# Kernel tuning notes

Measured on AMD Instinct MI355X. Metric: run time of the kernel, lower is better.

Reference implementation:

```python
import jax, jax.numpy as jnp
import numpy as np

DIM = 2048
NUM_HEADS = 16
HEAD_DIM = DIM // NUM_HEADS
HIDDEN = 4 * DIM
EPS = 1e-6


def rmsnorm(x, w):
    # Faithful to source: weight * (x * dim**-0.5 / sqrt(mean(x^2) + eps))
    scale = DIM ** -0.5
    norm = jnp.sqrt(jnp.mean(x * x, axis=-1, keepdims=True) + EPS)
    return w * (x * scale / norm)


def setup_inputs() -> dict:
    key = jax.random.key(0)
    ks = jax.random.split(key, 10)
    def init(k, shape, fan_in):
        return jax.random.normal(k, shape, dtype=jnp.float32) * (fan_in ** -0.5)
    return {
        "x": jax.random.normal(ks[0], (2, 2048, DIM), dtype=jnp.float32),
        "norm1_w": jnp.ones((DIM,), dtype=jnp.float32),
        "wq": init(ks[1], (DIM, DIM), DIM),
        "wk": init(ks[2], (HEAD_DIM, DIM), DIM),
        "wv": init(ks[3], (HEAD_DIM, DIM), DIM),
        "wo": init(ks[4], (DIM, DIM), DIM),
        "norm2_w": jnp.ones((DIM,), dtype=jnp.float32),
        "w1": init(ks[5], (HIDDEN, DIM), DIM),
        "w2": init(ks[6], (DIM, HIDDEN), HIDDEN),
        "w3": init(ks[7], (HIDDEN, DIM), DIM),
    }


def reference(x, norm1_w, wq, wk, wv, wo, norm2_w, w1, w2, w3):
    B, S, _ = x.shape
    # --- Multi-Query Attention (pre-norm) ---
    h = rmsnorm(x, norm1_w)
    q = h @ wq.T                                  # [B,S,D]
    k = h @ wk.T                                  # [B,S,hd] (shared across heads)
    v = h @ wv.T                                  # [B,S,hd]
    q = q.reshape(B, S, NUM_HEADS, HEAD_DIM)
    # scores: q @ k^T / sqrt(hd); k is broadcast (repeated) across heads
    scores = jnp.einsum('bshd,btd->bhst', q, k) / (HEAD_DIM ** 0.5)  # [B,H,S,S]
    probs = jax.nn.softmax(scores, axis=-1)
    attn = jnp.einsum('bhst,btd->bshd', probs, v).reshape(B, S, DIM)
    x = x + attn @ wo.T
    # --- SwiGLU FFN (pre-norm) ---
    h = rmsnorm(x, norm2_w)
    ffn = (jax.nn.silu(h @ w1.T) * (h @ w3.T)) @ w2.T
    return x + ffn
```

## Files before the change

kernel.cpp:

```cpp
#include <hip/hip_runtime.h>
#include <hip/hip_bf16.h>

typedef __attribute__((ext_vector_type(4))) float f32x4;
typedef __attribute__((ext_vector_type(8))) short s16x8;
typedef __attribute__((ext_vector_type(4))) short s16x4;
typedef __attribute__((ext_vector_type(2))) short s16x2;

#define MFMA_BF16 __builtin_amdgcn_mfma_f32_16x16x32_bf16

__device__ inline short f2bf(float f) {
  unsigned u = __float_as_uint(f);
  u = (u + 0x7FFFu + ((u >> 16) & 1u)) >> 16;
  return (short)u;
}
__device__ inline float bf2f(short s) {
  return __uint_as_float(((unsigned)(unsigned short)s) << 16);
}

#define DPPF(x, ctrl) __int_as_float(__builtin_amdgcn_update_dpp( \
    __float_as_int(x), __float_as_int(x), ctrl, 0xF, 0xF, false))
__device__ inline float rowmax16(float x) {
  x = fmaxf(x, DPPF(x, 0xB1));
  x = fmaxf(x, DPPF(x, 0x4E));
  x = fmaxf(x, DPPF(x, 0x124));
  x = fmaxf(x, DPPF(x, 0x128));
  return x;
}
__device__ inline float rowsum16(float x) {
  x += DPPF(x, 0xB1);
  x += DPPF(x, 0x4E);
  x += DPPF(x, 0x124);
  x += DPPF(x, 0x128);
  return x;
}

__global__ __launch_bounds__(256) void cvt_kernel(
    const float* __restrict__ in, short* __restrict__ out, int n, float scale)
{
  int idx = (blockIdx.x * 256 + threadIdx.x) * 8;
  if (idx >= n) return;
  f32x4 a = *(const f32x4*)(in + idx);
  f32x4 b = *(const f32x4*)(in + idx + 4);
  s16x8 o;
  #pragma unroll
  for (int j = 0; j < 4; ++j) { o[j] = f2bf(a[j] * scale); o[4 + j] = f2bf(b[j] * scale); }
  *(s16x8*)(out + idx) = o;
}

__global__ __launch_bounds__(256) void rmsnorm_kernel(
    const float* __restrict__ x, const float* __restrict__ w, short* __restrict__ out)
{
  size_t row = blockIdx.x;
  const float* xr = x + row * 2048;
  int base = threadIdx.x * 8;
  f32x4 a = *(const f32x4*)(xr + base);
  f32x4 b = *(const f32x4*)(xr + base + 4);
  float ss = a[0]*a[0] + a[1]*a[1] + a[2]*a[2] + a[3]*a[3]
           + b[0]*b[0] + b[1]*b[1] + b[2]*b[2] + b[3]*b[3];
  #pragma unroll
  for (int off = 1; off < 64; off <<= 1) ss += __shfl_xor(ss, off, 64);
  __shared__ float red[4];
  if ((threadIdx.x & 63) == 0) red[threadIdx.x >> 6] = ss;
  __syncthreads();
  float tot = red[0] + red[1] + red[2] + red[3];
  float rn = rsqrtf(tot * (1.0f / 2048.0f) + 1e-6f) * 0.022097086912079608f;
  f32x4 wa = *(const f32x4*)(w + base);
  f32x4 wb = *(const f32x4*)(w + base + 4);
  s16x8 o;
  #pragma unroll
  for (int j = 0; j < 4; ++j) {
    o[j]     = f2bf(a[j] * wa[j] * rn);
    o[4 + j] = f2bf(b[j] * wb[j] * rn);
  }
  *(s16x8*)(out + row * 2048 + base) = o;
}

template <int MODE>
__global__ __launch_bounds__(256, 2) void gemm_bt_kernel(
    const short* __restrict__ A, const short* __restrict__ B,
    void* __restrict__ Cv, const float* __restrict__ resid,
    int M, int N, int K)
{
  __shared__ short As[128 * 32];
  __shared__ short Bs[128 * 32];
  int tid = threadIdx.x;
  int lane = tid & 63;
  int w = tid >> 6;
  int r = lane & 15, g = lane >> 4;
  int wr = w >> 1, wc = w & 1;
  size_t row0 = (size_t)blockIdx.y * 128;
  size_t col0 = (size_t)blockIdx.x * 128;

  f32x4 acc[4][4];
  #pragma unroll
  for (int i = 0; i < 4; ++i)
    #pragma unroll
    for (int j = 0; j < 4; ++j) acc[i][j] = (f32x4){0.f, 0.f, 0.f, 0.f};

  const short* Ablk = A + row0 * K;
  const short* Bblk = B + col0 * K;
  int arow = tid >> 2;
  int akk = (tid & 3) << 3;

  for (int k0 = 0; k0 < K; k0 += 32) {
    #pragma unroll
    for (int i = 0; i < 2; ++i) {
      int chunk = i * 256 + tid;
      int rr = i * 64 + arow;
      __builtin_amdgcn_global_load_lds(
          (const __attribute__((address_space(1))) unsigned int*)(Ablk + (size_t)rr * K + k0 + akk),
          (__attribute__((address_space(3))) unsigned int*)(&As[chunk * 8]), 16, 0, 0);
      __builtin_amdgcn_global_load_lds(
          (const __attribute__((address_space(1))) unsigned int*)(Bblk + (size_t)rr * K + k0 + akk),
          (__attribute__((address_space(3))) unsigned int*)(&Bs[chunk * 8]), 16, 0, 0);
    }
    __syncthreads();
    s16x8 af[4], bfr[4];
    #pragma unroll
    for (int mm = 0; mm < 4; ++mm)
      af[mm] = *(const s16x8*)(&As[(wr * 64 + mm * 16 + r) * 32 + g * 8]);
    #pragma unroll
    for (int nn = 0; nn < 4; ++nn)
      bfr[nn] = *(const s16x8*)(&Bs[(wc * 64 + nn * 16 + r) * 32 + g * 8]);
    #pragma unroll
    for (int mm = 0; mm < 4; ++mm)
      #pragma unroll
      for (int nn = 0; nn < 4; ++nn)
        acc[mm][nn] = MFMA_BF16(af[mm], bfr[nn], acc[mm][nn], 0, 0, 0);
    __syncthreads();
  }

  #pragma unroll
  for (int mm = 0; mm < 4; ++mm) {
    #pragma unroll
    for (int nn = 0; nn < 4; ++nn) {
      #pragma unroll
      for (int j = 0; j < 4; ++j) {
        size_t rr = row0 + wr * 64 + mm * 16 + g * 4 + j;
        size_t cc = col0 + wc * 64 + nn * 16 + r;
        size_t idx = rr * (size_t)N + cc;
        if constexpr (MODE == 0) {
          ((short*)Cv)[idx] = f2bf(acc[mm][nn][j]);
        } else if constexpr (MODE == 1) {
          ((float*)Cv)[idx] = acc[mm][nn][j] + resid[idx];
        } else {
          short* gp = (short*)Cv;
          float gv = bf2f(gp[idx]);
          float sg = gv / (1.0f + __expf(-gv));
          gp[idx] = f2bf(sg * acc[mm][nn][j]);
        }
      }
    }
  }
}


#define STAGEA(T, KH)                                                          \
  _Pragma("unroll")                                                            \
  for (int i = 0; i < 2; ++i) {                                                \
    int lc = i * 512 + tid;                                                    \
    int rw = lc >> 2, cp = lc & 3;                                             \
    __builtin_amdgcn_global_load_lds(                                          \
        (const __attribute__((address_space(1))) unsigned int*)                \
            (Ablk + (size_t)rw * K + (T) * 64 + (KH) * 32 +                    \
             ((cp ^ ((rw >> 1) & 3)) << 3)),                                   \
        (__attribute__((address_space(3))) unsigned int*)                      \
            (&As[(T) & 1][KH][lc * 8]), 16, 0, 0);                             \
  }

#define STAGEB(T, KH)                                                          \
  _Pragma("unroll")                                                            \
  for (int i = 0; i < BLOADS; ++i) {                                           \
    int lc = i * 512 + tid;                                                    \
    int rw = lc >> 2, cp = lc & 3;                                             \
    __builtin_amdgcn_global_load_lds(                                          \
        (const __attribute__((address_space(1))) unsigned int*)                \
            (Bblk + (size_t)rw * K + (T) * 64 + (KH) * 32 +                    \
             ((cp ^ ((rw >> 1) & 3)) << 3)),                                   \
        (__attribute__((address_space(3))) unsigned int*)                      \
            (&Bs[(T) & 1][KH][lc * 8]), 16, 0, 0);                             \
  }

#define LDA8(D, KH, MH)                                                        \
  _Pragma("unroll")                                                            \
  for (int mi = 0; mi < 4; ++mi) {                                             \
    int rowa = wr * 128 + ((MH) * 4 + mi) * 16 + r;                            \
    a[mi] = *(const s16x8*)(&As[D][KH][rowa * 32 + chsw * 8]);                 \
  }

#define LDB8(D, KH)                                                            \
  _Pragma("unroll")                                                            \
  for (int ni = 0; ni < NREP; ++ni) {                                          \
    int rowb = wc * WN + ni * 16 + r;                                          \
    b[ni] = *(const s16x8*)(&Bs[D][KH][rowb * 32 + chsw * 8]);                 \
  }

#define MF16(MH)                                                               \
  __builtin_amdgcn_s_setprio(1);                                               \
  _Pragma("unroll")                                                            \
  for (int mi = 0; mi < 4; ++mi)                                               \
    _Pragma("unroll")                                                          \
    for (int ni = 0; ni < NREP; ++ni)                                          \
      acc[(MH) * 4 + mi][ni] =                                                 \
          MFMA_BF16(a[mi], b[ni], acc[(MH) * 4 + mi][ni], 0, 0, 0);            \
  __builtin_amdgcn_s_setprio(0);

#define WAITC                                                                  \
  do {                                                                         \
    if constexpr (BN == 256)                                                   \
      asm volatile("s_waitcnt vmcnt(4)" ::: "memory");                         \
    else                                                                       \
      asm volatile("s_waitcnt vmcnt(3)" ::: "memory");                         \
  } while (0)

#define BAR __builtin_amdgcn_s_barrier()

template <int BN, int MODE>
__global__ __launch_bounds__(512, 2) void gemm8p_kernel(
    const short* __restrict__ A, const short* __restrict__ B,
    void* __restrict__ Cv, const float* __restrict__ resid,
    int M, int N, int K)
{
  constexpr int BLOADS = BN / 128;
  constexpr int WN = BN / 4;
  constexpr int NREP = WN / 16;
  __shared__ short As[2][2][256 * 32];
  __shared__ short Bs[2][2][BN * 32];

  int tid = threadIdx.x;
  int lane = tid & 63;
  int w = tid >> 6;
  int r = lane & 15, g = lane >> 4;
  int wr = w >> 2, wc = w & 3;
  int chsw = g ^ ((r >> 1) & 3);

  int nwg = gridDim.x * gridDim.y;
  int orig = blockIdx.y * gridDim.x + blockIdx.x;
  int swz = (orig & 7) * (nwg >> 3) + (orig >> 3);
  int bx = swz % gridDim.x, by = swz / gridDim.x;
  size_t row0 = (size_t)by * 256;
  size_t col0 = (size_t)bx * BN;

  const short* Ablk = A + row0 * K;
  const short* Bblk = B + col0 * K;

  f32x4 acc[8][NREP];
  #pragma unroll
  for (int i = 0; i < 8; ++i)
    #pragma unroll
    for (int j = 0; j < NREP; ++j) acc[i][j] = (f32x4){0.f, 0.f, 0.f, 0.f};

  s16x8 a[4], b[NREP];
  int NT = K >> 6;

  STAGEA(0, 0); STAGEB(0, 0); STAGEA(0, 1); STAGEB(0, 1);
  WAITC;
  BAR;

  for (int t = 0; t < NT; ++t) {
    int d = t & 1;
    bool nl = (t < NT - 1);
    LDA8(d, 0, 0); LDB8(d, 0);
    if (nl) { STAGEA(t + 1, 0); }
    BAR;
    MF16(0);
    BAR;
    LDA8(d, 0, 1);
    if (nl) { STAGEB(t + 1, 0); WAITC; }
    else    { asm volatile("s_waitcnt vmcnt(0)" ::: "memory"); }
    BAR;
    MF16(1);
    BAR;
    LDA8(d, 1, 0); LDB8(d, 1);
    if (nl) { STAGEA(t + 1, 1); }
    BAR;
    MF16(0);
    BAR;
    LDA8(d, 1, 1);
    if (nl) { STAGEB(t + 1, 1); WAITC; }
    BAR;
    MF16(1);
    BAR;
  }

  #pragma unroll
  for (int mi = 0; mi < 8; ++mi) {
    #pragma unroll
    for (int ni = 0; ni < NREP; ++ni) {
      #pragma unroll
      for (int j = 0; j < 4; ++j) {
        size_t rr = row0 + wr * 128 + mi * 16 + g * 4 + j;
        size_t cc = col0 + wc * WN + ni * 16 + r;
        size_t idx = rr * (size_t)N + cc;
        if constexpr (MODE == 0) {
          ((short*)Cv)[idx] = f2bf(acc[mi][ni][j]);
        } else if constexpr (MODE == 1) {
          ((float*)Cv)[idx] = acc[mi][ni][j] + resid[idx];
        } else {
          short* gp = (short*)Cv;
          float gv = bf2f(gp[idx]);
          float sg = gv / (1.0f + __expf(-gv));
          gp[idx] = f2bf(sg * acc[mi][ni][j]);
        }
      }
    }
  }
}

__global__ __launch_bounds__(256) void transpose_v_kernel(
    const short* __restrict__ kv, short* __restrict__ vt)
{
  __shared__ short t[64][65];
  int b = blockIdx.z;
  int s0 = blockIdx.x * 64;
  int d0 = blockIdx.y * 64;
  int tid = threadIdx.x;
  #pragma unroll
  for (int i = 0; i < 16; ++i) {
    int e = i * 256 + tid;
    int sr = e >> 6, dc = e & 63;
    t[sr][dc] = kv[(size_t)(b * 2048 + s0 + sr) * 256 + 128 + d0 + dc];
  }
  __syncthreads();
  #pragma unroll
  for (int i = 0; i < 16; ++i) {
    int e = i * 256 + tid;
    int dr = e >> 6, sc = e & 63;
    vt[(size_t)b * 128 * 2048 + (size_t)(d0 + dr) * 2048 + s0 + sc] = t[sc][dr];
  }
}

__global__ __launch_bounds__(256, 2) void attn_kernel(
    const short* __restrict__ q, const short* __restrict__ kv,
    const short* __restrict__ vt, short* __restrict__ out)
{
  const int S = 2048;
  int tid = threadIdx.x;
  int w = tid >> 6;
  int lane = tid & 63;
  int r = lane & 15, g = lane >> 4;
  int h = blockIdx.y, b = blockIdx.z;
  int qrow0 = blockIdx.x * 128 + w * 32;

  __shared__ short Ks[2][4096];
  __shared__ short Vs[2][4096];
  __shared__ short Ps[4][32][40];

  const short* kvsrc = kv + (size_t)b * S * 256;
  const short* vsrc  = vt + (size_t)b * 128 * S;

  const short* qbase = q + ((size_t)(b * S + qrow0 + r)) * 2048 + h * 128;
  s16x8 qa[2][4];
  #pragma unroll
  for (int gq = 0; gq < 2; ++gq)
    #pragma unroll
    for (int dc = 0; dc < 4; ++dc)
      qa[gq][dc] = *(const s16x8*)(qbase + gq * 16 * 2048 + dc * 32 + g * 8);

  f32x4 o[2][8];
  #pragma unroll
  for (int gq = 0; gq < 2; ++gq)
    #pragma unroll
    for (int dt = 0; dt < 8; ++dt) o[gq][dt] = (f32x4){0.f, 0.f, 0.f, 0.f};
  float m[2][4], l[2][4];
  #pragma unroll
  for (int gq = 0; gq < 2; ++gq)
    #pragma unroll
    for (int j = 0; j < 4; ++j) { m[gq][j] = -1e30f; l[gq][j] = 0.f; }

#define STAGE(KVT, BSEL)                                                        \
  {                                                                             \
    int kv0s = (KVT) * 32;                                                      \
    _Pragma("unroll")                                                           \
    for (int i = 0; i < 2; ++i) {                                               \
      int c = w * 64 + lane + i * 256;                                          \
      int krow = c >> 4, kcp = c & 15;                                          \
      __builtin_amdgcn_global_load_lds(                                         \
          (const __attribute__((address_space(1))) unsigned int*)               \
              (kvsrc + (size_t)(kv0s + krow) * 256 + ((kcp ^ (krow & 7)) << 3)),\
          (__attribute__((address_space(3))) unsigned int*)(&Ks[BSEL][c * 8]),  \
          16, 0, 0);                                                            \
      int vrow = c >> 2, vcp = c & 3;                                           \
      __builtin_amdgcn_global_load_lds(                                         \
          (const __attribute__((address_space(1))) unsigned int*)               \
              (vsrc + (size_t)vrow * S + kv0s + ((vcp ^ (vrow & 3)) << 3)),     \
          (__attribute__((address_space(3))) unsigned int*)(&Vs[BSEL][c * 8]),  \
          16, 0, 0);                                                            \
    }                                                                           \
  }

  STAGE(0, 0);
  __syncthreads();

  for (int it = 0; it < 64; ++it) {
    int cur = it & 1;
    if (it < 63) STAGE(it + 1, cur ^ 1);

    s16x8 kc0[4], kc1[4], vb[8];
    #pragma unroll
    for (int dc = 0; dc < 4; ++dc) {
      kc0[dc] = *(const s16x8*)(&Ks[cur][r * 128 + (((dc * 4 + g) ^ (r & 7)) << 3)]);
      kc1[dc] = *(const s16x8*)(&Ks[cur][(16 + r) * 128 + (((dc * 4 + g) ^ (r & 7)) << 3)]);
    }
    #pragma unroll
    for (int dt = 0; dt < 8; ++dt)
      vb[dt] = *(const s16x8*)(&Vs[cur][(dt * 16 + r) * 32 + ((g ^ (r & 3)) << 3)]);

    f32x4 sc0[2], sc1[2];
    #pragma unroll
    for (int gq = 0; gq < 2; ++gq) { sc0[gq] = (f32x4){0.f,0.f,0.f,0.f}; sc1[gq] = (f32x4){0.f,0.f,0.f,0.f}; }
    __builtin_amdgcn_s_setprio(1);
    #pragma unroll
    for (int dc = 0; dc < 4; ++dc) {
      #pragma unroll
      for (int gq = 0; gq < 2; ++gq) {
        sc0[gq] = MFMA_BF16(qa[gq][dc], kc0[dc], sc0[gq], 0, 0, 0);
        sc1[gq] = MFMA_BF16(qa[gq][dc], kc1[dc], sc1[gq], 0, 0, 0);
      }
    }
    __builtin_amdgcn_s_setprio(0);

    float p0[2][4], p1[2][4];
    #pragma unroll
    for (int gq = 0; gq < 2; ++gq) {
      float mx[4];
      #pragma unroll
      for (int j = 0; j < 4; ++j) mx[j] = rowmax16(fmaxf(sc0[gq][j], sc1[gq][j]));
      bool nd = (mx[0] > m[gq][0] + 8.f) | (mx[1] > m[gq][1] + 8.f)
              | (mx[2] > m[gq][2] + 8.f) | (mx[3] > m[gq][3] + 8.f);
      if (__any(nd)) {
        #pragma unroll
        for (int j = 0; j < 4; ++j) {
          float mn = fmaxf(m[gq][j], mx[j]);
          float alpha = __expf(m[gq][j] - mn);
          m[gq][j] = mn;
          l[gq][j] *= alpha;
          #pragma unroll
          for (int dt = 0; dt < 8; ++dt) o[gq][dt][j] *= alpha;
        }
      }
      #pragma unroll
      for (int j = 0; j < 4; ++j) {
        p0[gq][j] = __expf(sc0[gq][j] - m[gq][j]);
        p1[gq][j] = __expf(sc1[gq][j] - m[gq][j]);
        l[gq][j] += p0[gq][j] + p1[gq][j];
      }
      #pragma unroll
      for (int j = 0; j < 4; ++j) {
        Ps[w][gq * 16 + g * 4 + j][r]      = f2bf(p0[gq][j]);
        Ps[w][gq * 16 + g * 4 + j][16 + r] = f2bf(p1[gq][j]);
      }
    }
    asm volatile("s_waitcnt lgkmcnt(0)" ::: "memory");
    __builtin_amdgcn_sched_barrier(0);
    s16x8 pa0 = *(const s16x8*)(&Ps[w][r][g * 8]);
    s16x8 pa1 = *(const s16x8*)(&Ps[w][16 + r][g * 8]);
    __builtin_amdgcn_s_setprio(1);
    #pragma unroll
    for (int dt = 0; dt < 8; ++dt) {
      o[0][dt] = MFMA_BF16(pa0, vb[dt], o[0][dt], 0, 0, 0);
      o[1][dt] = MFMA_BF16(pa1, vb[dt], o[1][dt], 0, 0, 0);
    }
    __builtin_amdgcn_s_setprio(0);
    __syncthreads();
  }

  #pragma unroll
  for (int gq = 0; gq < 2; ++gq) {
    float linv[4];
    #pragma unroll
    for (int j = 0; j < 4; ++j) linv[j] = 1.0f / rowsum16(l[gq][j]);
    short* ob = out + ((size_t)(b * S + qrow0 + gq * 16)) * 2048 + h * 128;
    #pragma unroll
    for (int dt = 0; dt < 8; ++dt)
      #pragma unroll
      for (int j = 0; j < 4; ++j)
        ob[(size_t)(g * 4 + j) * 2048 + dt * 16 + r] = f2bf(o[gq][dt][j] * linv[j]);
  }
#undef STAGE
}

extern "C" void kernel_launch(void* const* d_in, const int* in_sizes, int n_in,
                              void* d_out, int out_size, void* d_ws, size_t ws_size,
                              hipStream_t stream) {
  const float* x   = (const float*)d_in[0];
  const float* n1w = (const float*)d_in[1];
  const float* wq  = (const float*)d_in[2];
  const float* wk  = (const float*)d_in[3];
  const float* wv  = (const float*)d_in[4];
  const float* wo  = (const float*)d_in[5];
  const float* n2w = (const float*)d_in[6];
  const float* w1  = (const float*)d_in[7];
  const float* w2  = (const float*)d_in[8];
  const float* w3  = (const float*)d_in[9];
  float* out = (float*)d_out;
  char* ws = (char*)d_ws;
  const size_t MB = 1ull << 20;
  short* wqb  = (short*)(ws);
  short* wob  = (short*)(ws + 8 * MB);
  short* w1b  = (short*)(ws + 16 * MB);
  short* w2b  = (short*)(ws + 48 * MB);
  short* w3b  = (short*)(ws + 80 * MB);
  short* wkvb = (short*)(ws + 112 * MB);
  short* h1   = (short*)(ws + 113 * MB);
  short* gbuf = (short*)(ws + 129 * MB);
  short* qb   = (short*)(ws + 129 * MB);
  short* kvb  = (short*)(ws + 145 * MB);
  short* vtb  = (short*)(ws + 147 * MB);

  const float qscale = 0.08838834764831845f;
  cvt_kernel<<<2048, 256, 0, stream>>>(wq, wqb, 4194304, qscale);
  cvt_kernel<<<128,  256, 0, stream>>>(wk, wkvb, 262144, 1.0f);
  cvt_kernel<<<128,  256, 0, stream>>>(wv, wkvb + 262144, 262144, 1.0f);
  cvt_kernel<<<2048, 256, 0, stream>>>(wo, wob, 4194304, 1.0f);
  cvt_kernel<<<8192, 256, 0, stream>>>(w1, w1b, 16777216, 1.0f);
  cvt_kernel<<<8192, 256, 0, stream>>>(w2, w2b, 16777216, 1.0f);
  cvt_kernel<<<8192, 256, 0, stream>>>(w3, w3b, 16777216, 1.0f);

  rmsnorm_kernel<<<4096, 256, 0, stream>>>(x, n1w, h1);
  gemm8p_kernel<128, 0><<<dim3(16, 16), 512, 0, stream>>>(h1, wqb, qb, nullptr, 4096, 2048, 2048);
  gemm_bt_kernel<0><<<dim3(2, 32), 256, 0, stream>>>(h1, wkvb, kvb, nullptr, 4096, 256, 2048);
  transpose_v_kernel<<<dim3(32, 2, 2), 256, 0, stream>>>(kvb, vtb);
  attn_kernel<<<dim3(16, 16, 2), 256, 0, stream>>>(qb, kvb, vtb, h1);
  gemm8p_kernel<128, 1><<<dim3(16, 16), 512, 0, stream>>>(h1, wob, out, x, 4096, 2048, 2048);
  rmsnorm_kernel<<<4096, 256, 0, stream>>>(out, n2w, h1);
  gemm8p_kernel<256, 0><<<dim3(32, 16), 512, 0, stream>>>(h1, w1b, gbuf, nullptr, 4096, 8192, 2048);
  gemm8p_kernel<256, 2><<<dim3(32, 16), 512, 0, stream>>>(h1, w3b, gbuf, nullptr, 4096, 8192, 2048);
  gemm8p_kernel<128, 1><<<dim3(16, 16), 512, 0, stream>>>(gbuf, w2b, out, out, 4096, 2048, 8192);
}
```

Before: 897.6 us.

## Double-buffer LDS fragment registers to prefetch next MFMA operands

Splits the A and B fragment registers into two sets each, so the LDS reads for the next MFMA phase are issued before the current phase's MFMAs run. Operands for the next k-tile are prefetched at the end of each iteration, which removes the exposed LDS-read latency at the start of every phase. It raises VGPR pressure under the 512-thread, two-blocks-per-CU launch bounds. On the last iteration it also reads the other LDS buffer, which was never staged.

```diff
diff --git a/kernel.cpp b/kernel.cpp
--- a/kernel.cpp
+++ b/kernel.cpp
@@ -181,28 +181,28 @@
             (&Bs[(T) & 1][KH][lc * 8]), 16, 0, 0);                             \
   }
 
-#define LDA8(D, KH, MH)                                                        \
+#define LDA(SET, D, KH, MH)                                                    \
   _Pragma("unroll")                                                            \
   for (int mi = 0; mi < 4; ++mi) {                                             \
     int rowa = wr * 128 + ((MH) * 4 + mi) * 16 + r;                            \
-    a[mi] = *(const s16x8*)(&As[D][KH][rowa * 32 + chsw * 8]);                 \
-  }
-
-#define LDB8(D, KH)                                                            \
+    SET[mi] = *(const s16x8*)(&As[D][KH][rowa * 32 + chsw * 8]);               \
+  }
+
+#define LDB(SET, D, KH)                                                        \
   _Pragma("unroll")                                                            \
   for (int ni = 0; ni < NREP; ++ni) {                                          \
     int rowb = wc * WN + ni * 16 + r;                                          \
-    b[ni] = *(const s16x8*)(&Bs[D][KH][rowb * 32 + chsw * 8]);                 \
-  }
-
-#define MF16(MH)                                                               \
+    SET[ni] = *(const s16x8*)(&Bs[D][KH][rowb * 32 + chsw * 8]);               \
+  }
+
+#define MF(MH, ASET, BSET)                                                     \
   __builtin_amdgcn_s_setprio(1);                                               \
   _Pragma("unroll")                                                            \
   for (int mi = 0; mi < 4; ++mi)                                               \
     _Pragma("unroll")                                                          \
     for (int ni = 0; ni < NREP; ++ni)                                          \
       acc[(MH) * 4 + mi][ni] =                                                 \
-          MFMA_BF16(a[mi], b[ni], acc[(MH) * 4 + mi][ni], 0, 0, 0);            \
+          MFMA_BF16(ASET[mi], BSET[ni], acc[(MH) * 4 + mi][ni], 0, 0, 0);      \
   __builtin_amdgcn_s_setprio(0);
 
 #define WAITC                                                                  \
@@ -250,36 +250,40 @@
     #pragma unroll
     for (int j = 0; j < NREP; ++j) acc[i][j] = (f32x4){0.f, 0.f, 0.f, 0.f};
 
-  s16x8 a[4], b[NREP];
+  s16x8 aX[4], aY[4], bP[NREP], bQ[NREP];
   int NT = K >> 6;
 
   STAGEA(0, 0); STAGEB(0, 0); STAGEA(0, 1); STAGEB(0, 1);
   WAITC;
+  LDA(aX, 0, 0, 0);
+  LDB(bP, 0, 0);
   BAR;
 
   for (int t = 0; t < NT; ++t) {
     int d = t & 1;
     bool nl = (t < NT - 1);
-    LDA8(d, 0, 0); LDB8(d, 0);
+    LDA(aY, d, 0, 1);
     if (nl) { STAGEA(t + 1, 0); }
     BAR;
-    MF16(0);
-    BAR;
-    LDA8(d, 0, 1);
+    MF(0, aX, bP);
+    BAR;
     if (nl) { STAGEB(t + 1, 0); WAITC; }
     else    { asm volatile("s_waitcnt vmcnt(0)" ::: "memory"); }
-    BAR;
-    MF16(1);
-    BAR;
-    LDA8(d, 1, 0); LDB8(d, 1);
+    LDA(aX, d, 1, 0);
+    LDB(bQ, d, 1);
+    BAR;
+    MF(1, aY, bP);
+    BAR;
+    LDA(aY, d, 1, 1);
     if (nl) { STAGEA(t + 1, 1); }
     BAR;
-    MF16(0);
-    BAR;
-    LDA8(d, 1, 1);
+    MF(0, aX, bQ);
+    BAR;
     if (nl) { STAGEB(t + 1, 1); WAITC; }
-    BAR;
-    MF16(1);
+    LDA(aX, d ^ 1, 0, 0);
+    LDB(bP, d ^ 1, 0);
+    BAR;
+    MF(1, aY, bQ);
     BAR;
   }
 
```

New measurement: 988.4 us. 10.1% more time.

## Restructure GEMM main loop into two-phase schedule with full 64-wide K tiles

Applied to the files above, without the earlier changes.

Replaces the 8-phase GEMM pipeline, which split each 64-wide K tile into two 32-wide halves and staged A and B separately, with a 2-phase loop. The whole next K tile is issued up front, and all 8 A fragments are loaded per K-substep. The LDS layout becomes 64-element rows with an 8-way XOR swizzle. This cuts the number of barriers and waitcnts per tile, but it also loses the finer overlap of global loads with MFMA work and raises register pressure from holding 8 A fragments.

```diff
diff --git a/kernel.cpp b/kernel.cpp
--- a/kernel.cpp
+++ b/kernel.cpp
@@ -155,84 +155,71 @@
 }
 
 
-#define STAGEA(T, KH)                                                          \
+#define STAGEA2(T)                                                             \
   _Pragma("unroll")                                                            \
-  for (int i = 0; i < 2; ++i) {                                                \
+  for (int i = 0; i < 4; ++i) {                                                \
     int lc = i * 512 + tid;                                                    \
-    int rw = lc >> 2, cp = lc & 3;                                             \
+    int rw = lc >> 3, ch = lc & 7;                                             \
     __builtin_amdgcn_global_load_lds(                                          \
         (const __attribute__((address_space(1))) unsigned int*)                \
-            (Ablk + (size_t)rw * K + (T) * 64 + (KH) * 32 +                    \
-             ((cp ^ ((rw >> 1) & 3)) << 3)),                                   \
+            (Ablk + (size_t)rw * K + (T) * 64 + ((ch ^ (rw & 7)) << 3)),       \
         (__attribute__((address_space(3))) unsigned int*)                      \
-            (&As[(T) & 1][KH][lc * 8]), 16, 0, 0);                             \
-  }
-
-#define STAGEB(T, KH)                                                          \
+            (&As[(T) & 1][lc * 8]), 16, 0, 0);                                 \
+  }
+
+#define STAGEB2(T)                                                             \
   _Pragma("unroll")                                                            \
-  for (int i = 0; i < BLOADS; ++i) {                                           \
+  for (int i = 0; i < BLOADS2; ++i) {                                          \
     int lc = i * 512 + tid;                                                    \
-    int rw = lc >> 2, cp = lc & 3;                                             \
+    int rw = lc >> 3, ch = lc & 7;                                             \
     __builtin_amdgcn_global_load_lds(                                          \
         (const __attribute__((address_space(1))) unsigned int*)                \
-            (Bblk + (size_t)rw * K + (T) * 64 + (KH) * 32 +                    \
-             ((cp ^ ((rw >> 1) & 3)) << 3)),                                   \
+            (Bblk + (size_t)rw * K + (T) * 64 + ((ch ^ (rw & 7)) << 3)),       \
         (__attribute__((address_space(3))) unsigned int*)                      \
-            (&Bs[(T) & 1][KH][lc * 8]), 16, 0, 0);                             \
-  }
-
-#define LDA8(D, KH, MH)                                                        \
+            (&Bs[(T) & 1][lc * 8]), 16, 0, 0);                                 \
+  }
+
+#define LDALL(D, KS)                                                           \
   _Pragma("unroll")                                                            \
-  for (int mi = 0; mi < 4; ++mi) {                                             \
-    int rowa = wr * 128 + ((MH) * 4 + mi) * 16 + r;                            \
-    a[mi] = *(const s16x8*)(&As[D][KH][rowa * 32 + chsw * 8]);                 \
-  }
-
-#define LDB8(D, KH)                                                            \
+  for (int mi = 0; mi < 8; ++mi) {                                             \
+    int rowa = wr * 128 + mi * 16 + r;                                         \
+    aR[mi] = *(const s16x8*)(&As[D][rowa * 64 + ((((KS) * 4 + g) ^ (rowa & 7)) << 3)]); \
+  }                                                                            \
   _Pragma("unroll")                                                            \
   for (int ni = 0; ni < NREP; ++ni) {                                          \
     int rowb = wc * WN + ni * 16 + r;                                          \
-    b[ni] = *(const s16x8*)(&Bs[D][KH][rowb * 32 + chsw * 8]);                 \
-  }
-
-#define MF16(MH)                                                               \
+    bR[ni] = *(const s16x8*)(&Bs[D][rowb * 64 + ((((KS) * 4 + g) ^ (rowb & 7)) << 3)]); \
+  }
+
+#define MFALL                                                                  \
   __builtin_amdgcn_s_setprio(1);                                               \
   _Pragma("unroll")                                                            \
-  for (int mi = 0; mi < 4; ++mi)                                               \
+  for (int mi = 0; mi < 8; ++mi)                                               \
     _Pragma("unroll")                                                          \
     for (int ni = 0; ni < NREP; ++ni)                                          \
-      acc[(MH) * 4 + mi][ni] =                                                 \
-          MFMA_BF16(a[mi], b[ni], acc[(MH) * 4 + mi][ni], 0, 0, 0);            \
+      acc[mi][ni] = MFMA_BF16(aR[mi], bR[ni], acc[mi][ni], 0, 0, 0);           \
   __builtin_amdgcn_s_setprio(0);
 
-#define WAITC                                                                  \
-  do {                                                                         \
-    if constexpr (BN == 256)                                                   \
-      asm volatile("s_waitcnt vmcnt(4)" ::: "memory");                         \
-    else                                                                       \
-      asm volatile("s_waitcnt vmcnt(3)" ::: "memory");                         \
-  } while (0)
-
 #define BAR __builtin_amdgcn_s_barrier()
+#define VM0 asm volatile("s_waitcnt vmcnt(0)" ::: "memory")
 
 template <int BN, int MODE>
-__global__ __launch_bounds__(512, 2) void gemm8p_kernel(
+__global__ __launch_bounds__(512, 2) void gemm2p_kernel(
     const short* __restrict__ A, const short* __restrict__ B,
     void* __restrict__ Cv, const float* __restrict__ resid,
     int M, int N, int K)
 {
-  constexpr int BLOADS = BN / 128;
+  constexpr int BLOADS2 = BN / 64;
   constexpr int WN = BN / 4;
   constexpr int NREP = WN / 16;
-  __shared__ short As[2][2][256 * 32];
-  __shared__ short Bs[2][2][BN * 32];
+  __shared__ short As[2][256 * 64];
+  __shared__ short Bs[2][BN * 64];
 
   int tid = threadIdx.x;
   int lane = tid & 63;
   int w = tid >> 6;
   int r = lane & 15, g = lane >> 4;
   int wr = w >> 2, wc = w & 3;
-  int chsw = g ^ ((r >> 1) & 3);
 
   int nwg = gridDim.x * gridDim.y;
   int orig = blockIdx.y * gridDim.x + blockIdx.x;
@@ -250,36 +237,25 @@
     #pragma unroll
     for (int j = 0; j < NREP; ++j) acc[i][j] = (f32x4){0.f, 0.f, 0.f, 0.f};
 
-  s16x8 a[4], b[NREP];
+  s16x8 aR[8], bR[NREP];
   int NT = K >> 6;
 
-  STAGEA(0, 0); STAGEB(0, 0); STAGEA(0, 1); STAGEB(0, 1);
-  WAITC;
+  STAGEA2(0); STAGEB2(0);
+  VM0;
   BAR;
 
   for (int t = 0; t < NT; ++t) {
     int d = t & 1;
     bool nl = (t < NT - 1);
-    LDA8(d, 0, 0); LDB8(d, 0);
-    if (nl) { STAGEA(t + 1, 0); }
+    if (nl) { STAGEA2(t + 1); STAGEB2(t + 1); }
+    LDALL(d, 0);
     BAR;
-    MF16(0);
+    MFALL;
     BAR;
-    LDA8(d, 0, 1);
-    if (nl) { STAGEB(t + 1, 0); WAITC; }
-    else    { asm volatile("s_waitcnt vmcnt(0)" ::: "memory"); }
+    LDALL(d, 1);
+    VM0;
     BAR;
-    MF16(1);
-    BAR;
-    LDA8(d, 1, 0); LDB8(d, 1);
-    if (nl) { STAGEA(t + 1, 1); }
-    BAR;
-    MF16(0);
-    BAR;
-    LDA8(d, 1, 1);
-    if (nl) { STAGEB(t + 1, 1); WAITC; }
-    BAR;
-    MF16(1);
+    MFALL;
     BAR;
   }
 
@@ -518,13 +494,13 @@
   cvt_kernel<<<8192, 256, 0, stream>>>(w3, w3b, 16777216, 1.0f);
 
   rmsnorm_kernel<<<4096, 256, 0, stream>>>(x, n1w, h1);
-  gemm8p_kernel<128, 0><<<dim3(16, 16), 512, 0, stream>>>(h1, wqb, qb, nullptr, 4096, 2048, 2048);
+  gemm2p_kernel<128, 0><<<dim3(16, 16), 512, 0, stream>>>(h1, wqb, qb, nullptr, 4096, 2048, 2048);
   gemm_bt_kernel<0><<<dim3(2, 32), 256, 0, stream>>>(h1, wkvb, kvb, nullptr, 4096, 256, 2048);
   transpose_v_kernel<<<dim3(32, 2, 2), 256, 0, stream>>>(kvb, vtb);
   attn_kernel<<<dim3(16, 16, 2), 256, 0, stream>>>(qb, kvb, vtb, h1);
-  gemm8p_kernel<128, 1><<<dim3(16, 16), 512, 0, stream>>>(h1, wob, out, x, 4096, 2048, 2048);
+  gemm2p_kernel<128, 1><<<dim3(16, 16), 512, 0, stream>>>(h1, wob, out, x, 4096, 2048, 2048);
   rmsnorm_kernel<<<4096, 256, 0, stream>>>(out, n2w, h1);
-  gemm8p_kernel<256, 0><<<dim3(32, 16), 512, 0, stream>>>(h1, w1b, gbuf, nullptr, 4096, 8192, 2048);
-  gemm8p_kernel<256, 2><<<dim3(32, 16), 512, 0, stream>>>(h1, w3b, gbuf, nullptr, 4096, 8192, 2048);
-  gemm8p_kernel<128, 1><<<dim3(16, 16), 512, 0, stream>>>(gbuf, w2b, out, out, 4096, 2048, 8192);
-}
+  gemm2p_kernel<256, 0><<<dim3(32, 16), 512, 0, stream>>>(h1, w1b, gbuf, nullptr, 4096, 8192, 2048);
+  gemm2p_kernel<256, 2><<<dim3(32, 16), 512, 0, stream>>>(h1, w3b, gbuf, nullptr, 4096, 8192, 2048);
+  gemm2p_kernel<128, 1><<<dim3(16, 16), 512, 0, stream>>>(gbuf, w2b, out, out, 4096, 2048, 8192);
+}
```

New measurement: 967.6 us. +7.8%, slower.
